# Kernel tuning notes

Measured on AMD Instinct MI355X. Metric: run time of the kernel, lower is better.

Reference implementation:

```python
import jax, jax.numpy as jnp
import numpy as np

N_NODES = 50000
N_EDGES = 1600000
IN_CH = 128
HIDDEN = 128
N_CLASSES = 40


def setup_inputs() -> dict:
    key = jax.random.key(0)
    ks = jax.random.split(key, 8)
    node_features = jax.random.normal(ks[0], (1, N_NODES, IN_CH), dtype=jnp.float32)
    edge_index = jax.random.randint(ks[1], (1, 2, N_EDGES), 0, N_NODES, dtype=jnp.int64)
    rank_mapping = jnp.zeros((2, N_EDGES), dtype=jnp.int32)
    s1 = 1.0 / np.sqrt(IN_CH)
    s2 = 1.0 / np.sqrt(HIDDEN)
    W1 = jax.random.uniform(ks[2], (IN_CH, HIDDEN), jnp.float32, -s1, s1)
    b1 = jax.random.uniform(ks[3], (HIDDEN,), jnp.float32, -s1, s1)
    W2 = jax.random.uniform(ks[4], (HIDDEN, HIDDEN), jnp.float32, -s2, s2)
    b2 = jax.random.uniform(ks[5], (HIDDEN,), jnp.float32, -s2, s2)
    Wfc = jax.random.uniform(ks[6], (HIDDEN, N_CLASSES), jnp.float32, -s2, s2)
    bfc = jax.random.uniform(ks[7], (N_CLASSES,), jnp.float32, -s2, s2)
    return {"node_features": node_features, "edge_index": edge_index,
            "rank_mapping": rank_mapping, "W1": W1, "b1": b1,
            "W2": W2, "b2": b2, "Wfc": Wfc, "bfc": bfc}


def _gcn_single(feats, src, dst, W1, b1, W2, b2, Wfc, bfc):
    # feats: [N, F]; src/dst: [E]
    n = feats.shape[0]
    x = feats[dst]                                 # gather -> [E, F]
    x = jax.nn.relu(x @ W1 + b1)                   # conv1 (Linear + ReLU)
    x = jax.ops.segment_sum(x, src, num_segments=n)  # scatter-sum -> [N, H]
    x = x[dst]                                     # gather -> [E, H]
    x = x @ W2 + b2                                # conv2 (plain Linear)
    x = jax.ops.segment_sum(x, src, num_segments=n)  # scatter-sum -> [N, H]
    return x @ Wfc + bfc                           # [N, C]


def reference(node_features, edge_index, rank_mapping, W1, b1, W2, b2, Wfc, bfc):
    src = edge_index[:, 0, :]  # [B, E]
    dst = edge_index[:, 1, :]  # [B, E]
    return jax.vmap(_gcn_single, in_axes=(0, 0, 0, None, None, None, None, None, None))(
        node_features, src, dst, W1, b1, W2, b2, Wfc, bfc)
```

## Files before the change

kernel.cpp:

```cpp
#include <hip/hip_runtime.h>

static constexpr int NN = 50000;
static constexpr int NE = 1600000;
static constexpr int CH = 128;
static constexpr int NCLS = 40;

static constexpr int NPB  = 64;
static constexpr int NBUK = (NN + NPB - 1) / NPB;
static constexpr int NPB_SC = 256;
static constexpr int NBUK_SC = (NN + NPB_SC - 1) / NPB_SC;
static constexpr int EPB  = 8192;
static constexpr int NHB  = (NE + EPB - 1) / EPB;
static constexpr int NS   = NBUK_SC * NHB;
static constexpr int SCAN_B = 256;
static constexpr int SCAN_SHIFT = 8;
static constexpr int NSB  = (NS + SCAN_B - 1) / SCAN_B;
static constexpr int NROWP = ((NN + 63) / 64) * 64;
static constexpr int PAD = 136;
static constexpr int GEMM_BLKS = (NN + 63) / 64;
static constexpr int CAP = 3072;

typedef __attribute__((ext_vector_type(8))) short bf16x8;
typedef __attribute__((ext_vector_type(4))) float f32x4;

__device__ __forceinline__ float bflo(unsigned v) {
    return __uint_as_float((v & 0xFFFFu) << 16);
}
__device__ __forceinline__ float bfhi(unsigned v) {
    return __uint_as_float(v & 0xFFFF0000u);
}
__device__ __forceinline__ unsigned short f2bf(float f) {
    unsigned u = __float_as_uint(f);
    u += 0x7FFFu + ((u >> 16) & 1u);
    return (unsigned short)(u >> 16);
}

__global__ __launch_bounds__(256)
void fused_pre(const int* __restrict__ src, int* __restrict__ H,
               const float* __restrict__ W1, unsigned short* __restrict__ Wt_g,
               const float* __restrict__ W2, const float* __restrict__ Wfc,
               const float* __restrict__ b2, unsigned short* __restrict__ Mt,
               float* __restrict__ cfc)
{
    __shared__ int h[NBUK_SC];
    const int t = threadIdx.x;
    const int b = blockIdx.x;

    if (b < NHB) {
        for (int i = t; i < NBUK_SC; i += 256) h[i] = 0;
        __syncthreads();
        const int base4 = b * (EPB / 4);
        const int4* src4 = reinterpret_cast<const int4*>(src);
        for (int i = t; i < EPB / 4; i += 256) {
            const int idx = base4 + i;
            if (idx < NE / 4) {
                const int4 v = src4[idx];
                atomicAdd(&h[v.x >> 8], 1);
                atomicAdd(&h[v.y >> 8], 1);
                atomicAdd(&h[v.z >> 8], 1);
                atomicAdd(&h[v.w >> 8], 1);
            }
        }
        __syncthreads();
        for (int i = t; i < NBUK_SC; i += 256) H[i * NHB + b] = h[i];
    } else if (b < NHB + 64) {
        const int idx = (b - NHB) * 256 + t;
        const int c = idx >> 7;
        const int k = idx & 127;
        Wt_g[c * PAD + k] = f2bf(W1[k * 128 + c]);
    } else {
        const int idx = (b - NHB - 64) * 256 + t;
        if (idx < 48 * 128) {
            const int c = idx >> 7;
            const int k = idx & 127;
            float a = 0.f;
            if (c < NCLS) {
                #pragma unroll 16
                for (int j = 0; j < 128; ++j) a += W2[k * 128 + j] * Wfc[j * NCLS + c];
            }
            Mt[c * 128 + k] = f2bf(a);
        }
        if (b == NHB + 64 && t < NCLS) {
            float a = 0.f;
            #pragma unroll 16
            for (int j = 0; j < 128; ++j) a += b2[j] * Wfc[j * NCLS + t];
            cfc[t] = a;
        }
    }
}

__global__ __launch_bounds__(SCAN_B)
void scan_local(int* __restrict__ H, int* __restrict__ bsum)
{
    __shared__ int buf[SCAN_B];
    const int t = threadIdx.x;
    const int g = blockIdx.x * SCAN_B + t;
    const int v = (g < NS) ? H[g] : 0;
    buf[t] = v;
    __syncthreads();
    #pragma unroll
    for (int off = 1; off < SCAN_B; off <<= 1) {
        const int x = (t >= off) ? buf[t - off] : 0;
        __syncthreads();
        buf[t] += x;
        __syncthreads();
    }
    if (g < NS) H[g] = buf[t] - v;
    if (t == SCAN_B - 1) bsum[blockIdx.x] = buf[t];
}

__global__ __launch_bounds__(SCAN_B)
void scan_bsums(int* __restrict__ bsum)
{
    __shared__ int buf[SCAN_B];
    const int t = threadIdx.x;
    const int v = (t < NSB) ? bsum[t] : 0;
    buf[t] = v;
    __syncthreads();
    #pragma unroll
    for (int off = 1; off < SCAN_B; off <<= 1) {
        const int x = (t >= off) ? buf[t - off] : 0;
        __syncthreads();
        buf[t] += x;
        __syncthreads();
    }
    if (t < NSB) bsum[t] = buf[t] - v;
    if (t == SCAN_B - 1) bsum[NSB] = buf[t];
}

__global__ __launch_bounds__(256)
void fused_mid(const int* __restrict__ src, const int* __restrict__ dst,
               const int* __restrict__ H, const int* __restrict__ bsum,
               int* __restrict__ EP,
               const float* __restrict__ X, const unsigned short* __restrict__ Wt_g,
               const float* __restrict__ b, const unsigned short* __restrict__ Mt,
               unsigned short* __restrict__ V1)
{
    __shared__ __align__(16) unsigned short Wt[128 * PAD];
    __shared__ __align__(16) unsigned short Fa[64 * PAD];
    __shared__ __align__(16) unsigned short Va[64 * NCLS];
    __shared__ float bl[128];
    __shared__ int cur[NBUK_SC];

    const int t = threadIdx.x;

    if (blockIdx.x < NHB) {
        const int bb = blockIdx.x;
        for (int i = t; i < NBUK_SC; i += 256) {
            const int x = i * NHB + bb;
            cur[i] = H[x] + bsum[x >> SCAN_SHIFT];
        }
        __syncthreads();
        const int base4 = bb * (EPB / 4);
        const int4* src4 = reinterpret_cast<const int4*>(src);
        const int4* dst4 = reinterpret_cast<const int4*>(dst);
        for (int i = t; i < EPB / 4; i += 256) {
            const int idx = base4 + i;
            if (idx < NE / 4) {
                const int4 s4 = src4[idx];
                const int4 d4 = dst4[idx];
                int pos;
                pos = atomicAdd(&cur[s4.x >> 8], 1); EP[pos] = ((s4.x & 255) << 16) | d4.x;
                pos = atomicAdd(&cur[s4.y >> 8], 1); EP[pos] = ((s4.y & 255) << 16) | d4.y;
                pos = atomicAdd(&cur[s4.z >> 8], 1); EP[pos] = ((s4.z & 255) << 16) | d4.z;
                pos = atomicAdd(&cur[s4.w >> 8], 1); EP[pos] = ((s4.w & 255) << 16) | d4.w;
            }
        }
        return;
    }

    const int gb = blockIdx.x - NHB;
    const int lane = t & 63;
    const int w = t >> 6;

    for (int i = t; i < (128 * PAD) / 8; i += 256)
        reinterpret_cast<uint4*>(Wt)[i] = reinterpret_cast<const uint4*>(Wt_g)[i];
    if (t < 128) bl[t] = b[t];

    const int base = gb * 64;
    const int nRows = min(64, NN - base);
    {
        const int r = t >> 2;
        const int c0 = (t & 3) * 32;
        if (r < nRows) {
            #pragma unroll
            for (int j = 0; j < 32; j += 4) {
                const float4 v = *reinterpret_cast<const float4*>(&X[(size_t)(base + r) * CH + c0 + j]);
                ushort4 o; o.x = f2bf(v.x); o.y = f2bf(v.y); o.z = f2bf(v.z); o.w = f2bf(v.w);
                *reinterpret_cast<ushort4*>(&Fa[r * PAD + c0 + j]) = o;
            }
        } else {
            #pragma unroll
            for (int j = 0; j < 32; j += 4) {
                ushort4 z; z.x = z.y = z.z = z.w = 0;
                *reinterpret_cast<ushort4*>(&Fa[r * PAD + c0 + j]) = z;
            }
        }
    }
    __syncthreads();

    f32x4 acc[8];
    #pragma unroll
    for (int i = 0; i < 8; ++i) acc[i] = (f32x4){0.f, 0.f, 0.f, 0.f};

    const int arow = w * 16 + (lane & 15);
    const int kgrp = (lane >> 4) * 4;

    #pragma unroll
    for (int ks = 0; ks < 4; ++ks) {
        const int k0 = ks * 32 + kgrp;
        bf16x8 af;
        {
            const short4 lo = *reinterpret_cast<const short4*>(&Fa[arow * PAD + k0]);
            const short4 hi = *reinterpret_cast<const short4*>(&Fa[arow * PAD + k0 + 16]);
            af[0] = lo.x; af[1] = lo.y; af[2] = lo.z; af[3] = lo.w;
            af[4] = hi.x; af[5] = hi.y; af[6] = hi.z; af[7] = hi.w;
        }
        #pragma unroll
        for (int ct = 0; ct < 8; ++ct) {
            const int c = ct * 16 + (lane & 15);
            bf16x8 bf;
            const short4 lo = *reinterpret_cast<const short4*>(&Wt[c * PAD + k0]);
            const short4 hi = *reinterpret_cast<const short4*>(&Wt[c * PAD + k0 + 16]);
            bf[0] = lo.x; bf[1] = lo.y; bf[2] = lo.z; bf[3] = lo.w;
            bf[4] = hi.x; bf[5] = hi.y; bf[6] = hi.z; bf[7] = hi.w;
            acc[ct] = __builtin_amdgcn_mfma_f32_16x16x32_bf16(af, bf, acc[ct], 0, 0, 0);
        }
    }
    __syncthreads();

    #pragma unroll
    for (int ct = 0; ct < 8; ++ct) {
        const int c = ct * 16 + (lane & 15);
        const float bias = bl[c];
        #pragma unroll
        for (int r = 0; r < 4; ++r) {
            const int row = w * 16 + (lane >> 4) * 4 + r;
            Fa[row * PAD + c] = f2bf(fmaxf(acc[ct][r] + bias, 0.f));
        }
    }
    __syncthreads();

    f32x4 acc2[3];
    #pragma unroll
    for (int i = 0; i < 3; ++i) acc2[i] = (f32x4){0.f, 0.f, 0.f, 0.f};

    #pragma unroll
    for (int ks = 0; ks < 4; ++ks) {
        const int k0 = ks * 32 + kgrp;
        bf16x8 af;
        {
            const short4 lo = *reinterpret_cast<const short4*>(&Fa[arow * PAD + k0]);
            const short4 hi = *reinterpret_cast<const short4*>(&Fa[arow * PAD + k0 + 16]);
            af[0] = lo.x; af[1] = lo.y; af[2] = lo.z; af[3] = lo.w;
            af[4] = hi.x; af[5] = hi.y; af[6] = hi.z; af[7] = hi.w;
        }
        #pragma unroll
        for (int ct = 0; ct < 3; ++ct) {
            const int c = ct * 16 + (lane & 15);
            bf16x8 bf;
            const short4 lo = *reinterpret_cast<const short4*>(&Mt[c * 128 + k0]);
            const short4 hi = *reinterpret_cast<const short4*>(&Mt[c * 128 + k0 + 16]);
            bf[0] = lo.x; bf[1] = lo.y; bf[2] = lo.z; bf[3] = lo.w;
            bf[4] = hi.x; bf[5] = hi.y; bf[6] = hi.z; bf[7] = hi.w;
            acc2[ct] = __builtin_amdgcn_mfma_f32_16x16x32_bf16(af, bf, acc2[ct], 0, 0, 0);
        }
    }

    #pragma unroll
    for (int ct = 0; ct < 3; ++ct) {
        const int c = ct * 16 + (lane & 15);
        if (c < NCLS) {
            #pragma unroll
            for (int r = 0; r < 4; ++r) {
                const int row = w * 16 + (lane >> 4) * 4 + r;
                Va[row * NCLS + c] = f2bf(acc2[ct][r]);
            }
        }
    }
    __syncthreads();

    for (int i = t; i < 320; i += 256) {
        const int r = i / 5;
        const int q = i % 5;
        *reinterpret_cast<uint4*>(&V1[(size_t)(base + r) * NCLS + q * 8]) =
            *reinterpret_cast<const uint4*>(&Va[r * NCLS + q * 8]);
    }
}

__global__ __launch_bounds__(512)
void sortgather(const int* __restrict__ H, const int* __restrict__ bsum,
                const int* __restrict__ EP, const unsigned short* __restrict__ V1,
                unsigned short* __restrict__ U1, unsigned short* __restrict__ sdst,
                int* __restrict__ offs, int* __restrict__ deg)
{
    __shared__ int raw[CAP];
    __shared__ unsigned short srt[CAP];
    __shared__ int hist[NPB], cur[NPB], segBeg[NPB + 1];
    __shared__ int cnt;

    const int t = threadIdx.x;
    const int b = blockIdx.x;
    const int cb = b >> 2;
    const int sub = b & 3;
    const int node0 = b * NPB;
    const int nNodes = min(NPB, NN - node0);
    const int xb = cb * NHB;
    const int beg = H[xb] + bsum[xb >> SCAN_SHIFT];
    int end;
    if (cb == NBUK_SC - 1) end = NE;
    else { const int xe = (cb + 1) * NHB; end = H[xe] + bsum[xe >> SCAN_SHIFT]; }

    if (t == 0) cnt = 0;
    if (t < NPB) hist[t] = 0;
    __syncthreads();

    for (int i = beg + t; i < end; i += 512) {
        const int p = EP[i];
        const int hi = p >> 16;
        if ((hi >> 6) == sub) {
            const int pos = atomicAdd(&cnt, 1);
            raw[pos] = ((hi & 63) << 16) | (p & 0xFFFF);
        }
    }
    __syncthreads();
    const int C = cnt;

    for (int i = t; i < C; i += 512) atomicAdd(&hist[raw[i] >> 16], 1);
    __syncthreads();

    if (t < NPB) cur[t] = hist[t];
    __syncthreads();
    #pragma unroll
    for (int off = 1; off < NPB; off <<= 1) {
        int x = 0;
        if (t < NPB && t >= off) x = cur[t - off];
        __syncthreads();
        if (t < NPB) cur[t] += x;
        __syncthreads();
    }
    if (t < NPB) segBeg[t] = cur[t] - hist[t];
    if (t == 0) segBeg[NPB] = C;
    __syncthreads();

    if (t < nNodes) {
        offs[node0 + t] = b * CAP + segBeg[t];
        deg[node0 + t] = hist[t];
    }
    if (t < NPB) cur[t] = segBeg[t];
    __syncthreads();

    for (int i = t; i < C; i += 512) {
        const int p = raw[i];
        const int pos = atomicAdd(&cur[p >> 16], 1);
        srt[pos] = (unsigned short)(p & 0xFFFF);
    }
    __syncthreads();

    for (int i = t; i < C; i += 512) sdst[b * CAP + i] = srt[i];

    const int w = t >> 6;
    const int lane = t & 63;
    const int g = lane >> 4;
    const int L = lane & 15;

    for (int ni = 0; ni < 8; ++ni) {
        const int n = w * 8 + ni;
        if (n >= nNodes) break;
        const int sb = segBeg[n];
        const int se = segBeg[n + 1];
        float a0 = 0.f, a1 = 0.f, a2 = 0.f, a3 = 0.f;

        int i = sb;
        for (; i + 16 <= se; i += 16) {
            const int d0 = srt[i + g];
            const int d1 = srt[i + 4 + g];
            const int d2 = srt[i + 8 + g];
            const int d3 = srt[i + 12 + g];
            if (L < 10) {
                const uint2 v0 = *reinterpret_cast<const uint2*>(&V1[(size_t)d0 * NCLS + L * 4]);
                const uint2 v1 = *reinterpret_cast<const uint2*>(&V1[(size_t)d1 * NCLS + L * 4]);
                const uint2 v2 = *reinterpret_cast<const uint2*>(&V1[(size_t)d2 * NCLS + L * 4]);
                const uint2 v3 = *reinterpret_cast<const uint2*>(&V1[(size_t)d3 * NCLS + L * 4]);
                a0 += bflo(v0.x) + bflo(v1.x) + bflo(v2.x) + bflo(v3.x);
                a1 += bfhi(v0.x) + bfhi(v1.x) + bfhi(v2.x) + bfhi(v3.x);
                a2 += bflo(v0.y) + bflo(v1.y) + bflo(v2.y) + bflo(v3.y);
                a3 += bfhi(v0.y) + bfhi(v1.y) + bfhi(v2.y) + bfhi(v3.y);
            }
        }
        for (; i + 4 <= se; i += 4) {
            const int d = srt[i + g];
            if (L < 10) {
                const uint2 v = *reinterpret_cast<const uint2*>(&V1[(size_t)d * NCLS + L * 4]);
                a0 += bflo(v.x); a1 += bfhi(v.x);
                a2 += bflo(v.y); a3 += bfhi(v.y);
            }
        }
        const int rem = se - i;
        if (g < rem) {
            const int d = srt[i + g];
            if (L < 10) {
                const uint2 v = *reinterpret_cast<const uint2*>(&V1[(size_t)d * NCLS + L * 4]);
                a0 += bflo(v.x); a1 += bfhi(v.x);
                a2 += bflo(v.y); a3 += bfhi(v.y);
            }
        }

        a0 += __shfl_xor(a0, 16); a0 += __shfl_xor(a0, 32);
        a1 += __shfl_xor(a1, 16); a1 += __shfl_xor(a1, 32);
        a2 += __shfl_xor(a2, 16); a2 += __shfl_xor(a2, 32);
        a3 += __shfl_xor(a3, 16); a3 += __shfl_xor(a3, 32);

        if (lane < 16 && L < 10) {
            uint2 o;
            o.x = ((unsigned)f2bf(a1) << 16) | f2bf(a0);
            o.y = ((unsigned)f2bf(a3) << 16) | f2bf(a2);
            *reinterpret_cast<uint2*>(&U1[(size_t)(node0 + n) * NCLS + L * 4]) = o;
        }
    }
}

__global__ __launch_bounds__(512)
void gather40f(const int* __restrict__ offs, const unsigned short* __restrict__ sdst,
               const unsigned short* __restrict__ X, float* __restrict__ Yf,
               const int* __restrict__ deg,
               const float* __restrict__ cfc, const float* __restrict__ bfc)
{
    const int t = threadIdx.x;
    const int w = t >> 6;
    const int lane = t & 63;
    const int g = lane >> 4;
    const int L = lane & 15;
    const int node0 = blockIdx.x * 32 + w * 4;

    float4 cf = make_float4(0.f, 0.f, 0.f, 0.f);
    float4 bfv = make_float4(0.f, 0.f, 0.f, 0.f);
    if (L < 10) {
        cf  = *reinterpret_cast<const float4*>(&cfc[L * 4]);
        bfv = *reinterpret_cast<const float4*>(&bfc[L * 4]);
    }

    #pragma unroll
    for (int ni = 0; ni < 4; ++ni) {
        const int n = node0 + ni;
        if (n >= NN) break;
        const int sb = offs[n];
        const int dgi = deg[n];
        const int se = sb + dgi;
        float a0 = 0.f, a1 = 0.f, a2 = 0.f, a3 = 0.f;

        int i = sb;
        for (; i + 16 <= se; i += 16) {
            const int d0 = sdst[i + g];
            const int d1 = sdst[i + 4 + g];
            const int d2 = sdst[i + 8 + g];
            const int d3 = sdst[i + 12 + g];
            if (L < 10) {
                const uint2 v0 = *reinterpret_cast<const uint2*>(&X[(size_t)d0 * NCLS + L * 4]);
                const uint2 v1 = *reinterpret_cast<const uint2*>(&X[(size_t)d1 * NCLS + L * 4]);
                const uint2 v2 = *reinterpret_cast<const uint2*>(&X[(size_t)d2 * NCLS + L * 4]);
                const uint2 v3 = *reinterpret_cast<const uint2*>(&X[(size_t)d3 * NCLS + L * 4]);
                a0 += bflo(v0.x) + bflo(v1.x) + bflo(v2.x) + bflo(v3.x);
                a1 += bfhi(v0.x) + bfhi(v1.x) + bfhi(v2.x) + bfhi(v3.x);
                a2 += bflo(v0.y) + bflo(v1.y) + bflo(v2.y) + bflo(v3.y);
                a3 += bfhi(v0.y) + bfhi(v1.y) + bfhi(v2.y) + bfhi(v3.y);
            }
        }
        for (; i + 4 <= se; i += 4) {
            const int d = sdst[i + g];
            if (L < 10) {
                const uint2 v = *reinterpret_cast<const uint2*>(&X[(size_t)d * NCLS + L * 4]);
                a0 += bflo(v.x); a1 += bfhi(v.x);
                a2 += bflo(v.y); a3 += bfhi(v.y);
            }
        }
        const int rem = se - i;
        if (g < rem) {
            const int d = sdst[i + g];
            if (L < 10) {
                const uint2 v = *reinterpret_cast<const uint2*>(&X[(size_t)d * NCLS + L * 4]);
                a0 += bflo(v.x); a1 += bfhi(v.x);
                a2 += bflo(v.y); a3 += bfhi(v.y);
            }
        }

        a0 += __shfl_xor(a0, 16); a0 += __shfl_xor(a0, 32);
        a1 += __shfl_xor(a1, 16); a1 += __shfl_xor(a1, 32);
        a2 += __shfl_xor(a2, 16); a2 += __shfl_xor(a2, 32);
        a3 += __shfl_xor(a3, 16); a3 += __shfl_xor(a3, 32);

        if (lane < 16 && L < 10) {
            const float dgn = (float)dgi;
            float4 o;
            o.x = a0 + dgn * cf.x + bfv.x;
            o.y = a1 + dgn * cf.y + bfv.y;
            o.z = a2 + dgn * cf.z + bfv.z;
            o.w = a3 + dgn * cf.w + bfv.w;
            *reinterpret_cast<float4*>(&Yf[(size_t)n * NCLS + L * 4]) = o;
        }
    }
}

extern "C" void kernel_launch(void* const* d_in, const int* in_sizes, int n_in,
                              void* d_out, int out_size, void* d_ws, size_t ws_size,
                              hipStream_t stream) {
    const float* F   = (const float*)d_in[0];
    const int*   EI  = (const int*)  d_in[1];
    const float* W1  = (const float*)d_in[3];
    const float* b1  = (const float*)d_in[4];
    const float* W2  = (const float*)d_in[5];
    const float* b2  = (const float*)d_in[6];
    const float* Wfc = (const float*)d_in[7];
    const float* bfc = (const float*)d_in[8];
    float* out = (float*)d_out;

    char* ws = (char*)d_ws;
    size_t off = 0;
    auto take = [&](size_t bytes) { char* p = ws + off; off += (bytes + 63) & ~(size_t)63; return p; };

    unsigned short* V1   = (unsigned short*)take((size_t)NROWP * NCLS * 2);
    unsigned short* U1   = (unsigned short*)take((size_t)NROWP * NCLS * 2);
    unsigned short* sdst = (unsigned short*)take((size_t)NBUK * CAP * 2);
    int*   EP   = (int*)take((size_t)NE * 4);
    int*   H    = (int*)take((size_t)NS * 4);
    int*   bsum = (int*)take((size_t)(NSB + 1) * 4);
    int*   deg  = (int*)take((size_t)NN * 4);
    int*   offs = (int*)take((size_t)(NN + 1) * 4);
    unsigned short* Mt   = (unsigned short*)take((size_t)48 * 128 * 2);
    unsigned short* Wt_g = (unsigned short*)take((size_t)128 * PAD * 2);
    float* cfc  = (float*)take((size_t)NCLS * 4);

    const int* src = EI;
    const int* dst = EI + NE;

    fused_pre<<<NHB + 64 + 24, 256, 0, stream>>>(src, H, W1, Wt_g, W2, Wfc, b2, Mt, cfc);

    scan_local<<<NSB, SCAN_B, 0, stream>>>(H, bsum);
    scan_bsums<<<1, SCAN_B, 0, stream>>>(bsum);

    fused_mid<<<NHB + GEMM_BLKS, 256, 0, stream>>>(src, dst, H, bsum, EP,
                                                   F, Wt_g, b1, Mt, V1);

    sortgather<<<NBUK, 512, 0, stream>>>(H, bsum, EP, V1, U1, sdst, offs, deg);

    gather40f<<<(NN + 31) / 32, 512, 0, stream>>>(offs, sdst, U1, out, deg, cfc, bfc);
}
```

Baseline: 108.9 us.

## Replicate gather tables per XCC so random gathers hit local L2

Producer kernels now write eight copies of the bf16 V1 and U1 node tables, one per XCC. The consumer gather kernels read the XCC ID from a hardware register and use their local replica. The aim is to keep random gather traffic in each XCC's own L2 instead of sharing one copy across dies. In exchange the producers write eight times as many bytes and the workspace grows, and the gain depends on how the XCC caches behave.

```diff
diff --git a/kernel.cpp b/kernel.cpp
--- a/kernel.cpp
+++ b/kernel.cpp
@@ -19,6 +19,8 @@
 static constexpr int PAD = 136;
 static constexpr int GEMM_BLKS = (NN + 63) / 64;
 static constexpr int CAP = 3072;
+static constexpr size_t VSTRIDE = (size_t)NROWP * NCLS;
+static constexpr int NCOPY = 8;
 
 typedef __attribute__((ext_vector_type(8))) short bf16x8;
 typedef __attribute__((ext_vector_type(4))) float f32x4;
@@ -33,6 +35,11 @@
     unsigned u = __float_as_uint(f);
     u += 0x7FFFu + ((u >> 16) & 1u);
     return (unsigned short)(u >> 16);
+}
+__device__ __forceinline__ int xcc_id() {
+    int x;
+    asm volatile("s_getreg_b32 %0, hwreg(HW_REG_XCC_ID)" : "=s"(x));
+    return x & 7;
 }
 
 __global__ __launch_bounds__(256)
@@ -134,7 +141,7 @@
                int* __restrict__ EP,
                const float* __restrict__ X, const unsigned short* __restrict__ Wt_g,
                const float* __restrict__ b, const unsigned short* __restrict__ Mt,
-               unsigned short* __restrict__ V1)
+               unsigned short* __restrict__ V1R)
 {
     __shared__ __align__(16) unsigned short Wt[128 * PAD];
     __shared__ __align__(16) unsigned short Fa[64 * PAD];
@@ -280,18 +287,20 @@
     }
     __syncthreads();
 
-    for (int i = t; i < 320; i += 256) {
-        const int r = i / 5;
-        const int q = i % 5;
-        *reinterpret_cast<uint4*>(&V1[(size_t)(base + r) * NCLS + q * 8]) =
+    for (int i = t; i < 320 * NCOPY; i += 256) {
+        const int cp = i / 320;
+        const int j  = i % 320;
+        const int r = j / 5;
+        const int q = j % 5;
+        *reinterpret_cast<uint4*>(&V1R[(size_t)cp * VSTRIDE + (size_t)(base + r) * NCLS + q * 8]) =
             *reinterpret_cast<const uint4*>(&Va[r * NCLS + q * 8]);
     }
 }
 
 __global__ __launch_bounds__(512)
 void sortgather(const int* __restrict__ H, const int* __restrict__ bsum,
-                const int* __restrict__ EP, const unsigned short* __restrict__ V1,
-                unsigned short* __restrict__ U1, unsigned short* __restrict__ sdst,
+                const int* __restrict__ EP, const unsigned short* __restrict__ V1R,
+                unsigned short* __restrict__ U1R, unsigned short* __restrict__ sdst,
                 int* __restrict__ offs, int* __restrict__ deg)
 {
     __shared__ int raw[CAP];
@@ -310,6 +319,8 @@
     int end;
     if (cb == NBUK_SC - 1) end = NE;
     else { const int xe = (cb + 1) * NHB; end = H[xe] + bsum[xe >> SCAN_SHIFT]; }
+
+    const unsigned short* V1 = V1R + (size_t)xcc_id() * VSTRIDE;
 
     if (t == 0) cnt = 0;
     if (t < NPB) hist[t] = 0;
@@ -415,14 +426,17 @@
             uint2 o;
             o.x = ((unsigned)f2bf(a1) << 16) | f2bf(a0);
             o.y = ((unsigned)f2bf(a3) << 16) | f2bf(a2);
-            *reinterpret_cast<uint2*>(&U1[(size_t)(node0 + n) * NCLS + L * 4]) = o;
+            #pragma unroll
+            for (int cp = 0; cp < NCOPY; ++cp)
+                *reinterpret_cast<uint2*>(&U1R[(size_t)cp * VSTRIDE +
+                                               (size_t)(node0 + n) * NCLS + L * 4]) = o;
         }
     }
 }
 
 __global__ __launch_bounds__(512)
 void gather40f(const int* __restrict__ offs, const unsigned short* __restrict__ sdst,
-               const unsigned short* __restrict__ X, float* __restrict__ Yf,
+               const unsigned short* __restrict__ U1R, float* __restrict__ Yf,
                const int* __restrict__ deg,
                const float* __restrict__ cfc, const float* __restrict__ bfc)
 {
@@ -432,6 +446,8 @@
     const int g = lane >> 4;
     const int L = lane & 15;
     const int node0 = blockIdx.x * 32 + w * 4;
+
+    const unsigned short* X = U1R + (size_t)xcc_id() * VSTRIDE;
 
     float4 cf = make_float4(0.f, 0.f, 0.f, 0.f);
     float4 bfv = make_float4(0.f, 0.f, 0.f, 0.f);
@@ -518,8 +534,8 @@
     size_t off = 0;
     auto take = [&](size_t bytes) { char* p = ws + off; off += (bytes + 63) & ~(size_t)63; return p; };
 
-    unsigned short* V1   = (unsigned short*)take((size_t)NROWP * NCLS * 2);
-    unsigned short* U1   = (unsigned short*)take((size_t)NROWP * NCLS * 2);
+    unsigned short* V1R  = (unsigned short*)take(VSTRIDE * NCOPY * 2);
+    unsigned short* U1R  = (unsigned short*)take(VSTRIDE * NCOPY * 2);
     unsigned short* sdst = (unsigned short*)take((size_t)NBUK * CAP * 2);
     int*   EP   = (int*)take((size_t)NE * 4);
     int*   H    = (int*)take((size_t)NS * 4);
@@ -539,9 +555,9 @@
     scan_bsums<<<1, SCAN_B, 0, stream>>>(bsum);
 
     fused_mid<<<NHB + GEMM_BLKS, 256, 0, stream>>>(src, dst, H, bsum, EP,
-                                                   F, Wt_g, b1, Mt, V1);
-
-    sortgather<<<NBUK, 512, 0, stream>>>(H, bsum, EP, V1, U1, sdst, offs, deg);
-
-    gather40f<<<(NN + 31) / 32, 512, 0, stream>>>(offs, sdst, U1, out, deg, cfc, bfc);
-}
+                                                   F, Wt_g, b1, Mt, V1R);
+
+    sortgather<<<NBUK, 512, 0, stream>>>(H, bsum, EP, V1R, U1R, sdst, offs, deg);
+
+    gather40f<<<(NN + 31) / 32, 512, 0, stream>>>(offs, sdst, U1R, out, deg, cfc, bfc);
+}
```

Measured after the change: 125.7 us. 15.5% more time.
